# Optimization experiments

Hardware: AMD Instinct MI355X
Metric: run time of the kernel (lower is better)

The kernel has to match this reference:

```python
import jax, jax.numpy as jnp
import numpy as np

B = 8192
N_COLS = 64
D = 1024
EPS = 1e-5


def _layernorm(x, g, b):
    m = jnp.mean(x, axis=-1, keepdims=True)
    v = jnp.mean(jnp.square(x - m), axis=-1, keepdims=True)
    return (x - m) * jax.lax.rsqrt(v + EPS) * g + b


def setup_inputs() -> dict:
    key = jax.random.key(0)
    ks = jax.random.split(key, 8)
    s = 0.02
    return {
        "x1_enc": jax.random.normal(ks[0], (1, N_COLS, D), jnp.float32),
        "x2_enc": jax.random.normal(ks[1], (B, D), jnp.float32),
        "We": jax.random.normal(ks[2], (4, 2 * D, D), jnp.float32) * s,
        "be": jnp.zeros((4, D), jnp.float32),
        "W1": jax.random.normal(ks[3], (2 * D, 4 * D), jnp.float32) * s,
        "b1": jnp.zeros((4 * D,), jnp.float32),
        "g1": jnp.ones((4 * D,), jnp.float32),
        "bt1": jnp.zeros((4 * D,), jnp.float32),
        "W2": jax.random.normal(ks[4], (4 * D, 2 * D), jnp.float32) * s,
        "b2": jnp.zeros((2 * D,), jnp.float32),
        "g2": jnp.ones((2 * D,), jnp.float32),
        "bt2": jnp.zeros((2 * D,), jnp.float32),
        "W3": jax.random.normal(ks[5], (2 * D, 1), jnp.float32) * s,
        "b3": jnp.zeros((1,), jnp.float32),
        "col_pairs": jax.random.randint(ks[6], (B, 2), 0, N_COLS, jnp.int64),
        "vis_type": jax.random.randint(ks[7], (B,), 0, 4, jnp.int64),
    }


def reference(x1_enc, x2_enc, We, be, W1, b1, g1, bt1, W2, b2, g2, bt2, W3, b3,
              col_pairs, vis_type):
    # x1 repeated B times is identical per row -> gather directly from x1_enc[0]
    x11 = x1_enc[0, col_pairs[:, 0]]          # [B, D]
    x12 = x1_enc[0, col_pairs[:, 1]]          # [B, D]
    x1c = jnp.concatenate([x11, x12], axis=1)  # [B, 2D]

    # 1-of-4 expert routing: compute all experts, select by vis_type
    all_y = jax.nn.relu(jnp.einsum('bd,edk->bek', x1c, We) + be)  # [B, 4, D]
    y1 = jnp.take_along_axis(all_y, vis_type[:, None, None], axis=1)[:, 0]  # [B, D]

    y = jnp.concatenate([y1, x2_enc], axis=1)  # [B, 2D]
    h = _layernorm(jax.nn.relu(y @ W1 + b1), g1, bt1)
    h = _layernorm(jax.nn.relu(h @ W2 + b2), g2, bt2)
    return jax.nn.sigmoid(h @ W3 + b3)  # [B, 1]
```

## Files before the change

### kernel.cpp

```cpp
#include <hip/hip_runtime.h>

typedef unsigned short u16;
typedef __bf16 bf16x8 __attribute__((ext_vector_type(8)));
typedef float f32x4v __attribute__((ext_vector_type(4)));
typedef u16 u16x8 __attribute__((ext_vector_type(8)));

__device__ __forceinline__ u16 f2bf(float f) {
  union { float f; unsigned u; } v; v.f = f;
  unsigned r = v.u + 0x7fffu + ((v.u >> 16) & 1u);
  return (u16)(r >> 16);
}
__device__ __forceinline__ float bf2f(u16 h) {
  union { unsigned u; float f; } v; v.u = ((unsigned)h) << 16;
  return v.f;
}

#define G2L16(g, l)                                                            \
  __builtin_amdgcn_global_load_lds((__attribute__((address_space(1))) void*)(g), \
                                   (__attribute__((address_space(3))) void*)(l), 16, 0, 0)

__global__ __launch_bounds__(256) void k_prep(const float* __restrict__ W1,
                                              u16* __restrict__ W1T,
                                              const float* __restrict__ W2,
                                              u16* __restrict__ W2gT,
                                              const float* __restrict__ g1,
                                              const float* __restrict__ bt1,
                                              float* __restrict__ w2ps,
                                              float* __restrict__ w2pc,
                                              const float* __restrict__ x1,
                                              const float* __restrict__ We,
                                              float* __restrict__ pq) {
  __shared__ float lds[4224];
  int bid = blockIdx.x;
  const int t = threadIdx.x;
  if (bid < 4096) {
    float (*tile)[65] = (float(*)[65])lds;
    const float* in;
    u16* out;
    int R, C, bx, by, fold;
    if (bid < 2048) {
      in = W1; out = W1T; R = 2048; C = 4096; fold = 0;
      bx = bid & 63; by = bid >> 6;
    } else {
      bid -= 2048;
      in = W2; out = W2gT; R = 4096; C = 2048; fold = 1;
      bx = bid & 31; by = bid >> 5;
    }
    const int c0 = bx * 64, r0 = by * 64;
    const int tc = (t & 15) * 4, tr = t >> 4;
#pragma unroll
    for (int i = 0; i < 4; ++i) {
      int r = tr + i * 16;
      f32x4v v = *(const f32x4v*)(in + (size_t)(r0 + r) * C + c0 + tc);
      tile[r][tc] = v[0]; tile[r][tc + 1] = v[1];
      tile[r][tc + 2] = v[2]; tile[r][tc + 3] = v[3];
    }
    __syncthreads();
    const int oc = t >> 2;
    const int rb = (t & 3) * 16;
    float gv[16];
#pragma unroll
    for (int i = 0; i < 16; ++i) gv[i] = fold ? g1[r0 + rb + i] : 1.f;
    u16x8 o0, o1;
#pragma unroll
    for (int i = 0; i < 8; ++i) o0[i] = f2bf(tile[rb + i][oc] * gv[i]);
#pragma unroll
    for (int i = 0; i < 8; ++i) o1[i] = f2bf(tile[rb + 8 + i][oc] * gv[8 + i]);
    *(u16x8*)(out + (size_t)(c0 + oc) * R + r0 + rb) = o0;
    *(u16x8*)(out + (size_t)(c0 + oc) * R + r0 + rb + 8) = o1;
    if (fold) {
      float ps = 0.f, pc = 0.f;
#pragma unroll
      for (int i = 0; i < 16; ++i) {
        float w = tile[rb + i][oc];
        ps += gv[i] * w;
        pc += bt1[r0 + rb + i] * w;
      }
      ps += __shfl_down(ps, 2, 4); ps += __shfl_down(ps, 1, 4);
      pc += __shfl_down(pc, 2, 4); pc += __shfl_down(pc, 1, 4);
      if ((t & 3) == 0) {
        w2ps[(size_t)by * 2048 + c0 + oc] = ps;
        w2pc[(size_t)by * 2048 + c0 + oc] = pc;
      }
    }
  } else {
    const int pqb = bid - 4096;
    const int n0 = (pqb & 15) * 64;
    const int ep = (pqb >> 4) & 7;
    const int e = ep >> 1, p = ep & 1;
    const int chalf = pqb >> 7;
    float (*As)[33] = (float(*)[33])lds;
    float (*Bs)[68] = (float(*)[68])(lds + 32 * 33);
    const int tx = t & 15, ty = t >> 4;
    float acc[2][4] = {};
    const float* wbase = We + (size_t)e * 2048 * 1024 + (size_t)p * 1024 * 1024;
    for (int k0 = 0; k0 < 1024; k0 += 32) {
#pragma unroll
      for (int i = 0; i < 4; ++i) {
        int ix = t + i * 256;
        As[ix >> 5][ix & 31] =
            x1[(size_t)(chalf * 32 + (ix >> 5)) * 1024 + k0 + (ix & 31)];
      }
#pragma unroll
      for (int i = 0; i < 8; ++i) {
        int ix = t + i * 256;
        Bs[ix >> 6][ix & 63] = wbase[(size_t)(k0 + (ix >> 6)) * 1024 + n0 + (ix & 63)];
      }
      __syncthreads();
#pragma unroll
      for (int kk = 0; kk < 32; ++kk) {
        float av[2];
#pragma unroll
        for (int i = 0; i < 2; ++i) av[i] = As[ty * 2 + i][kk];
        f32x4v bv = *(const f32x4v*)&Bs[kk][tx * 4];
#pragma unroll
        for (int i = 0; i < 2; ++i)
#pragma unroll
          for (int j = 0; j < 4; ++j) acc[i][j] += av[i] * bv[j];
      }
      __syncthreads();
    }
#pragma unroll
    for (int i = 0; i < 2; ++i) {
      float* dst = pq + ((size_t)ep * 64 + chalf * 32 + ty * 2 + i) * 1024 + n0 + tx * 4;
#pragma unroll
      for (int j = 0; j < 4; ++j) dst[j] = acc[i][j];
    }
  }
}

__global__ __launch_bounds__(256) void k_build_y(const float* __restrict__ pq,
                                                 const float* __restrict__ x2,
                                                 const float* __restrict__ be,
                                                 const int* __restrict__ cp,
                                                 const int* __restrict__ vis,
                                                 u16* __restrict__ Y) {
  const int t = threadIdx.x;
  for (int rr = 0; rr < 8; ++rr) {
    const int b = blockIdx.x * 8 + rr;
    const int e = vis[b];
    u16x8 o;
    if (t < 128) {
      const int c0 = cp[2 * b], c1 = cp[2 * b + 1];
      const size_t po = ((size_t)(e * 2) * 64 + c0) * 1024 + t * 8;
      const size_t qo = ((size_t)(e * 2 + 1) * 64 + c1) * 1024 + t * 8;
      const float* B = be + e * 1024 + t * 8;
#pragma unroll
      for (int i = 0; i < 8; ++i) {
        float v = pq[po + i] + pq[qo + i] + B[i];
        o[i] = f2bf(v > 0.f ? v : 0.f);
      }
      *(u16x8*)(Y + (size_t)b * 2048 + t * 8) = o;
    } else {
      const float* X = x2 + (size_t)b * 1024 + (size_t)(t - 128) * 8;
#pragma unroll
      for (int i = 0; i < 8; ++i) o[i] = f2bf(X[i]);
      *(u16x8*)(Y + (size_t)b * 2048 + 1024 + (size_t)(t - 128) * 8) = o;
    }
  }
}

#define BARRIER __builtin_amdgcn_s_barrier()
#define WLG(n) asm volatile("s_waitcnt lgkmcnt(" #n ")" ::: "memory")
#define WVM(n) asm volatile("s_waitcnt vmcnt(" #n ")" ::: "memory")

template <int MODE>
__global__ __launch_bounds__(512, 2) void k_gemm(const u16* __restrict__ A,
                                                 const u16* __restrict__ BT,
                                                 const float* __restrict__ bias,
                                                 const float2* __restrict__ stats,
                                                 const float* __restrict__ s1,
                                                 const float* __restrict__ c1b,
                                                 const float* __restrict__ gw3,
                                                 float2* __restrict__ sp_out,
                                                 float4* __restrict__ part,
                                                 u16* __restrict__ C,
                                                 int M, int N, int K) {
  __shared__ u16 smem[65536];
  const int tid = threadIdx.x;
  const int lane = tid & 63;
  const int wave = tid >> 6;
  const int wm = wave >> 2;
  const int wn = wave & 3;

  const int nx = gridDim.x, ny = gridDim.y;
  const int bid = blockIdx.y * nx + blockIdx.x;
  const int stripe = ny >> 3;
  const int xcd = bid & 7;
  const int loc = bid >> 3;
  const int by = xcd * stripe + (loc % stripe);
  const int bx = loc / stripe;
  const int tileM = by * 256;
  const int tileN = bx * 256;

  f32x4v acc[8][4];
#pragma unroll
  for (int i = 0; i < 8; ++i)
#pragma unroll
    for (int j = 0; j < 4; ++j) acc[i][j] = (f32x4v){0.f, 0.f, 0.f, 0.f};

  const int srow = tid >> 3;
  const int slc = ((tid & 7) ^ (srow & 7)) * 8;
  const u16* aG = A + (size_t)(tileM + srow) * K + slc;
  const u16* bG = BT + (size_t)(tileN + srow) * K + slc;

#define STAGE(ab, h, buf, kt)                                                  \
  do {                                                                         \
    u16* dst_ = smem + (buf) * 32768 + (ab) * 16384 + (h) * 8192 + tid * 8;    \
    const u16* g_ = ((ab) ? bG : aG) + (size_t)(h) * 128 * K + (size_t)(kt) * 64; \
    G2L16(g_, dst_);                                                           \
    G2L16(g_ + (size_t)64 * K, dst_ + 4096);                                   \
  } while (0)

  const int kp0 = (((lane >> 4) ^ (lane & 7)) * 8);
  const int kp1 = kp0 ^ 32;
  const int awoff = wm * 8192 + (lane & 15) * 64;
  const int bwoff = (wn >> 1) * 8192 + ((wn & 1) * 64 + (lane & 15)) * 64;

  bf16x8 af[2][4], ag[2][4], bfr[2][4];

#define RD_AF(buf)                                                             \
  do {                                                                         \
    const u16* ap_ = smem + (buf) * 32768 + awoff;                             \
    _Pragma("unroll") for (int q = 0; q < 4; ++q) {                            \
      af[0][q] = *(const bf16x8*)(ap_ + q * 1024 + kp0);                       \
      af[1][q] = *(const bf16x8*)(ap_ + q * 1024 + kp1);                       \
    }                                                                          \
  } while (0)

#define RD_AG(buf)                                                             \
  do {                                                                         \
    const u16* ap_ = smem + (buf) * 32768 + awoff + 4096;                      \
    _Pragma("unroll") for (int q = 0; q < 4; ++q) {                            \
      ag[0][q] = *(const bf16x8*)(ap_ + q * 1024 + kp0);                       \
      ag[1][q] = *(const bf16x8*)(ap_ + q * 1024 + kp1);                       \
    }                                                                          \
  } while (0)

#define RD_BB(buf)                                                             \
  do {                                                                         \
    const u16* bp_ = smem + (buf) * 32768 + 16384 + bwoff;                     \
    _Pragma("unroll") for (int j = 0; j < 4; ++j) {                            \
      bfr[0][j] = *(const bf16x8*)(bp_ + j * 1024 + kp0);                      \
      bfr[1][j] = *(const bf16x8*)(bp_ + j * 1024 + kp1);                      \
    }                                                                          \
  } while (0)

#define QUAD(AF, mh, nh)                                                       \
  do {                                                                         \
    __builtin_amdgcn_s_setprio(1);                                             \
    _Pragma("unroll") for (int kh = 0; kh < 2; ++kh)                           \
    _Pragma("unroll") for (int q = 0; q < 4; ++q)                              \
    _Pragma("unroll") for (int p = 0; p < 2; ++p)                              \
      acc[(mh) * 4 + q][(nh) * 2 + p] = __builtin_amdgcn_mfma_f32_16x16x32_bf16( \
          AF[kh][q], bfr[(kh)][(nh) * 2 + p], acc[(mh) * 4 + q][(nh) * 2 + p], 0, 0, 0); \
    __builtin_amdgcn_s_setprio(0);                                             \
  } while (0)

  const int nkt = K >> 6;
  const int niter = nkt >> 1;

  STAGE(1, 0, 0, 0);
  STAGE(1, 1, 0, 0);
  STAGE(0, 0, 0, 0);
  STAGE(0, 1, 0, 0);
  STAGE(1, 0, 1, 1);
  STAGE(1, 1, 1, 1);
  WVM(4);

  for (int it = 0; it < niter; ++it) {
    const int t1 = 2 * it + 1;
    int t2 = 2 * it + 2; if (t2 >= nkt) t2 = nkt - 1;
    int t3 = 2 * it + 3; if (t3 >= nkt) t3 = nkt - 1;
    BARRIER;
    RD_AF(0); RD_BB(0);
    STAGE(0, 0, 1, t1);
    WLG(4);
    QUAD(af, 0, 0);
    BARRIER;
    RD_AG(0);
    STAGE(0, 1, 1, t1);
    WLG(8);
    QUAD(af, 0, 1);
    BARRIER;
    STAGE(1, 0, 0, t2);
    WLG(0);
    QUAD(ag, 1, 0);
    BARRIER;
    STAGE(1, 1, 0, t2);
    QUAD(ag, 1, 1);
    WVM(4);
    BARRIER;
    RD_AF(1); RD_BB(1);
    STAGE(0, 0, 0, t2);
    WLG(4);
    QUAD(af, 0, 0);
    BARRIER;
    RD_AG(1);
    STAGE(0, 1, 0, t2);
    WLG(8);
    QUAD(af, 0, 1);
    BARRIER;
    STAGE(1, 0, 1, t3);
    WLG(0);
    QUAD(ag, 1, 0);
    BARRIER;
    STAGE(1, 1, 1, t3);
    QUAD(ag, 1, 1);
    WVM(4);
  }

  const int crow = tileM + wm * 128 + (lane >> 4) * 4;
  const int ccol = tileN + wn * 64 + (lane & 15);
  float cv0[4], cv1[4], cg[4];
#pragma unroll
  for (int ni = 0; ni < 4; ++ni) {
    const int c = ccol + ni * 16;
    if (MODE == 0) {
      cv0[ni] = bias[c];
    } else {
      cv0[ni] = s1[c];
      cv1[ni] = c1b[c];
      cg[ni] = gw3[c];
    }
  }
  const int cb = bx * 4 + wn;
#pragma unroll
  for (int mi = 0; mi < 8; ++mi) {
#pragma unroll
    for (int r = 0; r < 4; ++r) {
      const int row = crow + mi * 16 + r;
      if (MODE == 0) {
        float s_ = 0.f, ss_ = 0.f;
#pragma unroll
        for (int ni = 0; ni < 4; ++ni) {
          float v = acc[mi][ni][r] + cv0[ni];
          v = v > 0.f ? v : 0.f;
          s_ += v; ss_ += v * v;
          C[(size_t)row * N + ccol + ni * 16] = f2bf(v);
        }
#pragma unroll
        for (int off = 8; off >= 1; off >>= 1) {
          s_ += __shfl_xor(s_, off, 16);
          ss_ += __shfl_xor(ss_, off, 16);
        }
        if ((lane & 15) == 0)
          sp_out[(size_t)row * 64 + cb] = make_float2(s_, ss_);
      } else {
        float2 st = stats[row];
        const float m = st.x, rs = st.y;
        float s_ = 0.f, ss_ = 0.f, d_ = 0.f;
#pragma unroll
        for (int ni = 0; ni < 4; ++ni) {
          float v = rs * acc[mi][ni][r] - rs * m * cv0[ni] + cv1[ni];
          v = v > 0.f ? v : 0.f;
          s_ += v; ss_ += v * v; d_ += v * cg[ni];
        }
#pragma unroll
        for (int off = 8; off >= 1; off >>= 1) {
          s_ += __shfl_xor(s_, off, 16);
          ss_ += __shfl_xor(ss_, off, 16);
          d_ += __shfl_xor(d_, off, 16);
        }
        if ((lane & 15) == 0)
          part[(size_t)row * 32 + cb] = make_float4(s_, ss_, d_, 0.f);
      }
    }
  }
}

__global__ __launch_bounds__(256) void k_reduce(const float2* __restrict__ sp,
                                                float2* __restrict__ stats,
                                                const float* __restrict__ w2ps,
                                                const float* __restrict__ w2pc,
                                                const float* __restrict__ b2,
                                                float* __restrict__ s1,
                                                float* __restrict__ c1b,
                                                const float* __restrict__ g2,
                                                const float* __restrict__ bt2,
                                                const float* __restrict__ W3,
                                                float* __restrict__ gw3,
                                                float* __restrict__ scal) {
  __shared__ float red[8];
  const int bid = blockIdx.x;
  const int t = threadIdx.x;
  if (bid < 32) {
    const int g = t >> 4, l = t & 15;
#pragma unroll 1
    for (int rr = 0; rr < 16; ++rr) {
      const int row = bid * 256 + rr * 16 + g;
      float s = 0.f, ss = 0.f;
#pragma unroll
      for (int i = 0; i < 4; ++i) {
        float2 p = sp[(size_t)row * 64 + l * 4 + i];
        s += p.x; ss += p.y;
      }
#pragma unroll
      for (int off = 8; off >= 1; off >>= 1) {
        s += __shfl_xor(s, off, 16);
        ss += __shfl_xor(ss, off, 16);
      }
      if (l == 0) {
        float m = s * (1.f / 4096.f);
        float var = ss * (1.f / 4096.f) - m * m;
        stats[row] = make_float2(m, rsqrtf(var + 1e-5f));
      }
    }
  } else if (bid < 40) {
    const int nn = (bid - 32) * 256 + t;
    float s = 0.f, c = 0.f;
    for (int kb = 0; kb < 64; ++kb) {
      s += w2ps[(size_t)kb * 2048 + nn];
      c += w2pc[(size_t)kb * 2048 + nn];
    }
    s1[nn] = s;
    c1b[nn] = c + b2[nn];
  } else {
    float sg = 0.f, cb = 0.f;
    for (int i = 0; i < 8; ++i) {
      int c = i * 256 + t;
      float w3 = W3[c];
      float gv = g2[c] * w3;
      gw3[c] = gv;
      sg += gv;
      cb += bt2[c] * w3;
    }
#pragma unroll
    for (int off = 32; off > 0; off >>= 1) {
      sg += __shfl_down(sg, off, 64);
      cb += __shfl_down(cb, off, 64);
    }
    const int lane = t & 63, wv = t >> 6;
    if (lane == 0) { red[wv] = sg; red[4 + wv] = cb; }
    __syncthreads();
    if (t == 0) {
      scal[0] = red[0] + red[1] + red[2] + red[3];
      scal[1] = red[4] + red[5] + red[6] + red[7];
    }
  }
}

__global__ __launch_bounds__(256) void k_final(const float4* __restrict__ part,
                                               const float* __restrict__ scal,
                                               const float* __restrict__ b3,
                                               float* __restrict__ out) {
  const int t = threadIdx.x;
  const int g = t >> 4, l = t & 15;
  const int row = blockIdx.x * 16 + g;
  float4 a = part[(size_t)row * 32 + l * 2];
  float4 b = part[(size_t)row * 32 + l * 2 + 1];
  float S = a.x + b.x, SS = a.y + b.y, D = a.z + b.z;
#pragma unroll
  for (int off = 8; off >= 1; off >>= 1) {
    S += __shfl_xor(S, off, 16);
    SS += __shfl_xor(SS, off, 16);
    D += __shfl_xor(D, off, 16);
  }
  if (l == 0) {
    float m = S * (1.f / 2048.f);
    float rs = rsqrtf(SS * (1.f / 2048.f) - m * m + 1e-5f);
    float logit = rs * D - rs * m * scal[0] + scal[1] + b3[0];
    out[row] = 1.f / (1.f + expf(-logit));
  }
}

extern "C" void kernel_launch(void* const* d_in, const int* in_sizes, int n_in,
                              void* d_out, int out_size, void* d_ws, size_t ws_size,
                              hipStream_t stream) {
  const float* x1 = (const float*)d_in[0];
  const float* x2 = (const float*)d_in[1];
  const float* We = (const float*)d_in[2];
  const float* be = (const float*)d_in[3];
  const float* W1 = (const float*)d_in[4];
  const float* b1 = (const float*)d_in[5];
  const float* g1 = (const float*)d_in[6];
  const float* bt1 = (const float*)d_in[7];
  const float* W2 = (const float*)d_in[8];
  const float* b2 = (const float*)d_in[9];
  const float* g2 = (const float*)d_in[10];
  const float* bt2 = (const float*)d_in[11];
  const float* W3 = (const float*)d_in[12];
  const float* b3 = (const float*)d_in[13];
  const int* cp = (const int*)d_in[14];
  const int* vis = (const int*)d_in[15];
  float* out = (float*)d_out;

  char* ws = (char*)d_ws;
  u16* W1T  = (u16*)(ws);
  u16* W2gT = (u16*)(ws + 16777216);
  u16* Y    = (u16*)(ws + 33554432);
  u16* H1   = (u16*)(ws + 67108864);
  float* PQ = (float*)(ws + 134217728);
  float2* sp = (float2*)(ws + 134217728);
  float4* part = (float4*)(ws + 134217728);
  float2* stats = (float2*)(ws + 138412032);
  float* s1   = (float*)(ws + 138477568);
  float* c1b  = (float*)(ws + 138485760);
  float* w2ps = (float*)(ws + 138493952);
  float* w2pc = (float*)(ws + 139018240);
  float* gw3  = (float*)(ws + 139542528);
  float* scal = (float*)(ws + 139550720);

  k_prep<<<4352, 256, 0, stream>>>(W1, W1T, W2, W2gT, g1, bt1, w2ps, w2pc,
                                   x1, We, PQ);
  k_build_y<<<1024, 256, 0, stream>>>(PQ, x2, be, cp, vis, Y);
  k_gemm<0><<<dim3(16, 32), 512, 0, stream>>>(
      Y, W1T, b1, nullptr, nullptr, nullptr, nullptr, sp, nullptr, H1,
      8192, 4096, 2048);
  k_reduce<<<41, 256, 0, stream>>>(sp, stats, w2ps, w2pc, b2, s1, c1b,
                                   g2, bt2, W3, gw3, scal);
  k_gemm<1><<<dim3(8, 32), 512, 0, stream>>>(
      H1, W2gT, nullptr, stats, s1, c1b, gw3, nullptr, part, nullptr,
      8192, 2048, 4096);
  k_final<<<512, 256, 0, stream>>>(part, scal, b3, out);
}
```

Baseline: 454.2 us.

## Replace partial-sum buffers and reduce kernel with atomic row accumulation

```diff
diff --git a/kernel.cpp b/kernel.cpp
--- a/kernel.cpp
+++ b/kernel.cpp
@@ -134,28 +134,86 @@
                                                  const float* __restrict__ be,
                                                  const int* __restrict__ cp,
                                                  const int* __restrict__ vis,
-                                                 u16* __restrict__ Y) {
+                                                 u16* __restrict__ Y,
+                                                 const float* __restrict__ w2ps,
+                                                 const float* __restrict__ w2pc,
+                                                 const float* __restrict__ b2,
+                                                 float* __restrict__ s1,
+                                                 float* __restrict__ c1b,
+                                                 const float* __restrict__ g2,
+                                                 const float* __restrict__ bt2,
+                                                 const float* __restrict__ W3,
+                                                 float* __restrict__ gw3,
+                                                 float* __restrict__ scal,
+                                                 float* __restrict__ ssum,
+                                                 float* __restrict__ rowacc) {
+  __shared__ float red[8];
   const int t = threadIdx.x;
-  for (int rr = 0; rr < 8; ++rr) {
-    const int b = blockIdx.x * 8 + rr;
-    const int e = vis[b];
-    u16x8 o;
-    if (t < 128) {
-      const int c0 = cp[2 * b], c1 = cp[2 * b + 1];
-      const size_t po = ((size_t)(e * 2) * 64 + c0) * 1024 + t * 8;
-      const size_t qo = ((size_t)(e * 2 + 1) * 64 + c1) * 1024 + t * 8;
-      const float* B = be + e * 1024 + t * 8;
-#pragma unroll
+  const int bidx = blockIdx.x;
+  if (bidx < 1024) {
+    for (int rr = 0; rr < 8; ++rr) {
+      const int b = bidx * 8 + rr;
+      const int e = vis[b];
+      u16x8 o;
+      if (t < 128) {
+        const int c0 = cp[2 * b], c1 = cp[2 * b + 1];
+        const size_t po = ((size_t)(e * 2) * 64 + c0) * 1024 + t * 8;
+        const size_t qo = ((size_t)(e * 2 + 1) * 64 + c1) * 1024 + t * 8;
+        const float* B = be + e * 1024 + t * 8;
+#pragma unroll
+        for (int i = 0; i < 8; ++i) {
+          float v = pq[po + i] + pq[qo + i] + B[i];
+          o[i] = f2bf(v > 0.f ? v : 0.f);
+        }
+        *(u16x8*)(Y + (size_t)b * 2048 + t * 8) = o;
+      } else {
+        const float* X = x2 + (size_t)b * 1024 + (size_t)(t - 128) * 8;
+#pragma unroll
+        for (int i = 0; i < 8; ++i) o[i] = f2bf(X[i]);
+        *(u16x8*)(Y + (size_t)b * 2048 + 1024 + (size_t)(t - 128) * 8) = o;
+      }
+    }
+  } else {
+    const int r = bidx - 1024;
+    if (r < 8) {
+      const int nn = r * 256 + t;
+      float s = 0.f, c = 0.f;
+      for (int kb = 0; kb < 64; ++kb) {
+        s += w2ps[(size_t)kb * 2048 + nn];
+        c += w2pc[(size_t)kb * 2048 + nn];
+      }
+      s1[nn] = s;
+      c1b[nn] = c + b2[nn];
+    } else if (r == 8) {
+      float sg = 0.f, cb = 0.f;
       for (int i = 0; i < 8; ++i) {
-        float v = pq[po + i] + pq[qo + i] + B[i];
-        o[i] = f2bf(v > 0.f ? v : 0.f);
-      }
-      *(u16x8*)(Y + (size_t)b * 2048 + t * 8) = o;
+        int c = i * 256 + t;
+        float w3 = W3[c];
+        float gv = g2[c] * w3;
+        gw3[c] = gv;
+        sg += gv;
+        cb += bt2[c] * w3;
+      }
+#pragma unroll
+      for (int off = 32; off > 0; off >>= 1) {
+        sg += __shfl_down(sg, off, 64);
+        cb += __shfl_down(cb, off, 64);
+      }
+      const int lane = t & 63, wv = t >> 6;
+      if (lane == 0) { red[wv] = sg; red[4 + wv] = cb; }
+      __syncthreads();
+      if (t == 0) {
+        scal[0] = red[0] + red[1] + red[2] + red[3];
+        scal[1] = red[4] + red[5] + red[6] + red[7];
+      }
+    } else if (r == 9) {
+      float4* p = (float4*)ssum;
+#pragma unroll 4
+      for (int i = t; i < 4096; i += 256) p[i] = make_float4(0.f, 0.f, 0.f, 0.f);
     } else {
-      const float* X = x2 + (size_t)b * 1024 + (size_t)(t - 128) * 8;
-#pragma unroll
-      for (int i = 0; i < 8; ++i) o[i] = f2bf(X[i]);
-      *(u16x8*)(Y + (size_t)b * 2048 + 1024 + (size_t)(t - 128) * 8) = o;
+      float4* p = (float4*)rowacc + (r - 10) * 4096;
+#pragma unroll 4
+      for (int i = t; i < 4096; i += 256) p[i] = make_float4(0.f, 0.f, 0.f, 0.f);
     }
   }
 }
@@ -172,8 +230,8 @@
                                                  const float* __restrict__ s1,
                                                  const float* __restrict__ c1b,
                                                  const float* __restrict__ gw3,
-                                                 float2* __restrict__ sp_out,
-                                                 float4* __restrict__ part,
+                                                 float* __restrict__ ssum,
+                                                 float* __restrict__ rowacc,
                                                  u16* __restrict__ C,
                                                  int M, int N, int K) {
   __shared__ u16 smem[65536];
@@ -324,7 +382,6 @@
       cg[ni] = gw3[c];
     }
   }
-  const int cb = bx * 4 + wn;
 #pragma unroll
   for (int mi = 0; mi < 8; ++mi) {
 #pragma unroll
@@ -344,11 +401,14 @@
           s_ += __shfl_xor(s_, off, 16);
           ss_ += __shfl_xor(ss_, off, 16);
         }
-        if ((lane & 15) == 0)
-          sp_out[(size_t)row * 64 + cb] = make_float2(s_, ss_);
+        if ((lane & 15) == 0) {
+          atomicAdd(ssum + (size_t)row * 2, s_);
+          atomicAdd(ssum + (size_t)row * 2 + 1, ss_);
+        }
       } else {
-        float2 st = stats[row];
-        const float m = st.x, rs = st.y;
+        float2 sv = stats[row];
+        const float m = sv.x * (1.f / 4096.f);
+        const float rs = rsqrtf(sv.y * (1.f / 4096.f) - m * m + 1e-5f);
         float s_ = 0.f, ss_ = 0.f, d_ = 0.f;
 #pragma unroll
         for (int ni = 0; ni < 4; ++ni) {
@@ -362,106 +422,26 @@
           ss_ += __shfl_xor(ss_, off, 16);
           d_ += __shfl_xor(d_, off, 16);
         }
-        if ((lane & 15) == 0)
-          part[(size_t)row * 32 + cb] = make_float4(s_, ss_, d_, 0.f);
+        if ((lane & 15) == 0) {
+          atomicAdd(rowacc + (size_t)row * 4, s_);
+          atomicAdd(rowacc + (size_t)row * 4 + 1, ss_);
+          atomicAdd(rowacc + (size_t)row * 4 + 2, d_);
+        }
       }
     }
   }
 }
 
-__global__ __launch_bounds__(256) void k_reduce(const float2* __restrict__ sp,
-                                                float2* __restrict__ stats,
-                                                const float* __restrict__ w2ps,
-                                                const float* __restrict__ w2pc,
-                                                const float* __restrict__ b2,
-                                                float* __restrict__ s1,
-                                                float* __restrict__ c1b,
-                                                const float* __restrict__ g2,
-                                                const float* __restrict__ bt2,
-                                                const float* __restrict__ W3,
-                                                float* __restrict__ gw3,
-                                                float* __restrict__ scal) {
-  __shared__ float red[8];
-  const int bid = blockIdx.x;
-  const int t = threadIdx.x;
-  if (bid < 32) {
-    const int g = t >> 4, l = t & 15;
-#pragma unroll 1
-    for (int rr = 0; rr < 16; ++rr) {
-      const int row = bid * 256 + rr * 16 + g;
-      float s = 0.f, ss = 0.f;
-#pragma unroll
-      for (int i = 0; i < 4; ++i) {
-        float2 p = sp[(size_t)row * 64 + l * 4 + i];
-        s += p.x; ss += p.y;
-      }
-#pragma unroll
-      for (int off = 8; off >= 1; off >>= 1) {
-        s += __shfl_xor(s, off, 16);
-        ss += __shfl_xor(ss, off, 16);
-      }
-      if (l == 0) {
-        float m = s * (1.f / 4096.f);
-        float var = ss * (1.f / 4096.f) - m * m;
-        stats[row] = make_float2(m, rsqrtf(var + 1e-5f));
-      }
-    }
-  } else if (bid < 40) {
-    const int nn = (bid - 32) * 256 + t;
-    float s = 0.f, c = 0.f;
-    for (int kb = 0; kb < 64; ++kb) {
-      s += w2ps[(size_t)kb * 2048 + nn];
-      c += w2pc[(size_t)kb * 2048 + nn];
-    }
-    s1[nn] = s;
-    c1b[nn] = c + b2[nn];
-  } else {
-    float sg = 0.f, cb = 0.f;
-    for (int i = 0; i < 8; ++i) {
-      int c = i * 256 + t;
-      float w3 = W3[c];
-      float gv = g2[c] * w3;
-      gw3[c] = gv;
-      sg += gv;
-      cb += bt2[c] * w3;
-    }
-#pragma unroll
-    for (int off = 32; off > 0; off >>= 1) {
-      sg += __shfl_down(sg, off, 64);
-      cb += __shfl_down(cb, off, 64);
-    }
-    const int lane = t & 63, wv = t >> 6;
-    if (lane == 0) { red[wv] = sg; red[4 + wv] = cb; }
-    __syncthreads();
-    if (t == 0) {
-      scal[0] = red[0] + red[1] + red[2] + red[3];
-      scal[1] = red[4] + red[5] + red[6] + red[7];
-    }
-  }
-}
-
-__global__ __launch_bounds__(256) void k_final(const float4* __restrict__ part,
+__global__ __launch_bounds__(256) void k_final(const float4* __restrict__ rowacc,
                                                const float* __restrict__ scal,
                                                const float* __restrict__ b3,
                                                float* __restrict__ out) {
-  const int t = threadIdx.x;
-  const int g = t >> 4, l = t & 15;
-  const int row = blockIdx.x * 16 + g;
-  float4 a = part[(size_t)row * 32 + l * 2];
-  float4 b = part[(size_t)row * 32 + l * 2 + 1];
-  float S = a.x + b.x, SS = a.y + b.y, D = a.z + b.z;
-#pragma unroll
-  for (int off = 8; off >= 1; off >>= 1) {
-    S += __shfl_xor(S, off, 16);
-    SS += __shfl_xor(SS, off, 16);
-    D += __shfl_xor(D, off, 16);
-  }
-  if (l == 0) {
-    float m = S * (1.f / 2048.f);
-    float rs = rsqrtf(SS * (1.f / 2048.f) - m * m + 1e-5f);
-    float logit = rs * D - rs * m * scal[0] + scal[1] + b3[0];
-    out[row] = 1.f / (1.f + expf(-logit));
-  }
+  const int row = blockIdx.x * 256 + threadIdx.x;
+  float4 a = rowacc[row];
+  float m = a.x * (1.f / 2048.f);
+  float rs = rsqrtf(a.y * (1.f / 2048.f) - m * m + 1e-5f);
+  float logit = rs * a.z - rs * m * scal[0] + scal[1] + b3[0];
+  out[row] = 1.f / (1.f + expf(-logit));
 }
 
 extern "C" void kernel_launch(void* const* d_in, const int* in_sizes, int n_in,
@@ -491,26 +471,25 @@
   u16* Y    = (u16*)(ws + 33554432);
   u16* H1   = (u16*)(ws + 67108864);
   float* PQ = (float*)(ws + 134217728);
-  float2* sp = (float2*)(ws + 134217728);
-  float4* part = (float4*)(ws + 134217728);
-  float2* stats = (float2*)(ws + 138412032);
-  float* s1   = (float*)(ws + 138477568);
-  float* c1b  = (float*)(ws + 138485760);
-  float* w2ps = (float*)(ws + 138493952);
-  float* w2pc = (float*)(ws + 139018240);
-  float* gw3  = (float*)(ws + 139542528);
-  float* scal = (float*)(ws + 139550720);
+  float* ssum   = (float*)(ws + 138412032);
+  float* rowacc = (float*)(ws + 138477568);
+  float* s1   = (float*)(ws + 138608640);
+  float* c1b  = (float*)(ws + 138616832);
+  float* w2ps = (float*)(ws + 138625024);
+  float* w2pc = (float*)(ws + 139149312);
+  float* gw3  = (float*)(ws + 139673600);
+  float* scal = (float*)(ws + 139681792);
 
   k_prep<<<4352, 256, 0, stream>>>(W1, W1T, W2, W2gT, g1, bt1, w2ps, w2pc,
                                    x1, We, PQ);
-  k_build_y<<<1024, 256, 0, stream>>>(PQ, x2, be, cp, vis, Y);
+  k_build_y<<<1036, 256, 0, stream>>>(PQ, x2, be, cp, vis, Y,
+                                      w2ps, w2pc, b2, s1, c1b,
+                                      g2, bt2, W3, gw3, scal, ssum, rowacc);
   k_gemm<0><<<dim3(16, 32), 512, 0, stream>>>(
-      Y, W1T, b1, nullptr, nullptr, nullptr, nullptr, sp, nullptr, H1,
+      Y, W1T, b1, nullptr, nullptr, nullptr, nullptr, ssum, nullptr, H1,
       8192, 4096, 2048);
-  k_reduce<<<41, 256, 0, stream>>>(sp, stats, w2ps, w2pc, b2, s1, c1b,
-                                   g2, bt2, W3, gw3, scal);
   k_gemm<1><<<dim3(8, 32), 512, 0, stream>>>(
-      H1, W2gT, nullptr, stats, s1, c1b, gw3, nullptr, part, nullptr,
-      8192, 2048, 4096);
-  k_final<<<512, 256, 0, stream>>>(part, scal, b3, out);
-}
+      H1, W2gT, nullptr, (const float2*)ssum, s1, c1b, gw3, nullptr, rowacc,
+      nullptr, 8192, 2048, 4096);
+  k_final<<<32, 256, 0, stream>>>((const float4*)rowacc, scal, b3, out);
+}
```

Result: slower. 580.9 us (+27.9%).
